# Performance work log

Measured on AMD Instinct MI355X. Metric: run time of the kernel, lower is better.

## Reference

```python
import jax, jax.numpy as jnp
import numpy as np

HEADS = 16
DIM_HEAD = 64
QUERY_DIM = 1024
CONTEXT_DIM = 1024
D_ATTN = HEADS * DIM_HEAD
SCALE = DIM_HEAD ** -0.5


def setup_inputs() -> dict:
    key = jax.random.key(0)
    ks = jax.random.split(key, 7)
    B, N, M = 4, 2048, 1024
    x = jax.random.normal(ks[0], (B, N, QUERY_DIM), dtype=jnp.float32)
    context = jax.random.normal(ks[1], (B, M, CONTEXT_DIM), dtype=jnp.float32)
    # Linear weights stored as [in, out] (no bias for Q/K/V, bias for to_out)
    s = 0.02
    Wq = jax.random.normal(ks[2], (QUERY_DIM, D_ATTN), dtype=jnp.float32) * s
    Wk = jax.random.normal(ks[3], (CONTEXT_DIM, D_ATTN), dtype=jnp.float32) * s
    Wv = jax.random.normal(ks[4], (CONTEXT_DIM, D_ATTN), dtype=jnp.float32) * s
    Wo = jax.random.normal(ks[5], (D_ATTN, QUERY_DIM), dtype=jnp.float32) * s
    bo = jax.random.normal(ks[6], (QUERY_DIM,), dtype=jnp.float32) * s
    return {"x": x, "context": context, "Wq": Wq, "Wk": Wk, "Wv": Wv, "Wo": Wo, "bo": bo}


def reference(x, context, Wq, Wk, Wv, Wo, bo):
    B, N, _ = x.shape
    M = context.shape[1]
    Q = (x @ Wq).reshape(B, N, HEADS, DIM_HEAD)        # b n h d
    K = (context @ Wk).reshape(B, M, HEADS, DIM_HEAD)  # b m h d
    V = (context @ Wv).reshape(B, M, HEADS, DIM_HEAD)
    # scores: b q h m  (matches torch einsum 'bqhd,bhmd->bqhm')
    scores = jnp.einsum('bqhd,bmhd->bqhm', Q, K) * SCALE
    attn = jax.nn.softmax(scores, axis=-1)
    out = jnp.einsum('bqhm,bmhd->bqhd', attn, V)
    out = out.reshape(B, N, D_ATTN)
    return out @ Wo + bo  # dropout p=0.0 -> identity
```

## Files before the change

### kernel.cpp

```cpp
#include <hip/hip_runtime.h>
#include <math.h>


#define HEADS 16
#define DHEAD 64
#define DM    1024
#define BQ    4
#define NQ    2048
#define MK    1024

typedef unsigned short u16;
typedef __attribute__((ext_vector_type(8))) short bf16x8;
typedef __attribute__((ext_vector_type(4))) float f32x4;
typedef __attribute__((ext_vector_type(16))) float f32x16;

__device__ __forceinline__ u16 f2bf(float f) {
  unsigned u = __builtin_bit_cast(unsigned, f);
  u = u + 0x7FFFu + ((u >> 16) & 1u);
  return (u16)(u >> 16);
}

__device__ __forceinline__ unsigned cvtpk(float lo, float hi2) {
  unsigned r;
  asm("v_cvt_pk_bf16_f32 %0, %1, %2" : "=v"(r) : "v"(lo), "v"(hi2));
  return r;
}

__device__ __forceinline__ float max3f(float a, float b, float c) {
  float d;
  asm("v_max3_f32 %0, %1, %2, %3" : "=v"(d) : "v"(a), "v"(b), "v"(c));
  return d;
}

__device__ __forceinline__ void gld16(const u16* g, u16* l) {
  __builtin_amdgcn_global_load_lds((const __attribute__((address_space(1))) void*)g,
                                   (__attribute__((address_space(3))) void*)l,
                                   16, 0, 0);
}

__global__ void k_cvt(const float* __restrict__ in, u16* __restrict__ out, int n8) {
  int i = blockIdx.x * 256 + threadIdx.x;
  if (i >= n8) return;
  float4 a = ((const float4*)in)[i * 2];
  float4 b = ((const float4*)in)[i * 2 + 1];
  union { u16 h[8]; int4 v; } r;
  r.h[0] = f2bf(a.x); r.h[1] = f2bf(a.y); r.h[2] = f2bf(a.z); r.h[3] = f2bf(a.w);
  r.h[4] = f2bf(b.x); r.h[5] = f2bf(b.y); r.h[6] = f2bf(b.z); r.h[7] = f2bf(b.w);
  ((int4*)out)[i] = r.v;
}

__global__ void k_wt(const float* __restrict__ W0, const float* __restrict__ W1,
                     const float* __restrict__ W2, const float* __restrict__ W3,
                     u16* __restrict__ out) {
  __shared__ float t[32][33];
  const float* W = blockIdx.z == 0 ? W0 : blockIdx.z == 1 ? W1 : blockIdx.z == 2 ? W2 : W3;
  u16* o = out + (size_t)blockIdx.z * DM * DM;
  int r0 = blockIdx.y * 32, c0 = blockIdx.x * 32;
  int tx = threadIdx.x, ty = threadIdx.y;
  for (int i = ty; i < 32; i += 8) t[i][tx] = W[(size_t)(r0 + i) * DM + c0 + tx];
  __syncthreads();
  for (int i = ty; i < 32; i += 8) o[(size_t)(c0 + i) * DM + r0 + tx] = f2bf(t[tx][i]);
}


#define VM6 asm volatile("s_waitcnt vmcnt(6)" ::: "memory")

#define STAGE_A8(bufi, h, kof) do {                                          \
  gld16(gA + (size_t)(h) * 131072 + (kof), &As8[bufi][(h) * 8192 + w * 512]); \
  gld16(gA + (size_t)(h) * 131072 + 65536 + (kof),                           \
        &As8[bufi][(h) * 8192 + 4096 + w * 512]);                            \
} while (0)

#define STAGE_B8(bufi, h, kof) do {                                          \
  gld16(gB + (size_t)(h) * 131072 + (kof), &Bs8[bufi][(h) * 8192 + w * 512]); \
  gld16(gB + (size_t)(h) * 131072 + 65536 + (kof),                           \
        &Bs8[bufi][(h) * 8192 + 4096 + w * 512]);                            \
} while (0)

#define RD_A8(qm) do { _Pragma("unroll")                                     \
  for (int mi = 0; mi < 4; ++mi) {                                           \
    const u16* pa = &As8[cur][((qm) * 128 + wmo + mi * 16 + lrow) * 64];     \
    af8[mi][0] = *(const bf16x8*)(pa + fo0);                                 \
    af8[mi][1] = *(const bf16x8*)(pa + (fo0 ^ 32));                          \
  } } while (0)

#define RD_B8(qn) do { _Pragma("unroll")                                     \
  for (int ni = 0; ni < 2; ++ni) {                                           \
    const u16* pb = &Bs8[cur][((qn) * 128 + wno + ni * 16 + lrow) * 64];     \
    bf8[ni][0] = *(const bf16x8*)(pb + fo0);                                 \
    bf8[ni][1] = *(const bf16x8*)(pb + (fo0 ^ 32));                          \
  } } while (0)

#define MM16(qm, qn) do {                                                    \
  __builtin_amdgcn_s_setprio(1);                                             \
  _Pragma("unroll")                                                          \
  for (int mi = 0; mi < 4; ++mi)                                             \
    _Pragma("unroll")                                                        \
    for (int ni = 0; ni < 2; ++ni) {                                         \
      acc[qm][qn][mi][ni] = __builtin_amdgcn_mfma_f32_16x16x32_bf16(         \
          af8[mi][0], bf8[ni][0], acc[qm][qn][mi][ni], 0, 0, 0);             \
      acc[qm][qn][mi][ni] = __builtin_amdgcn_mfma_f32_16x16x32_bf16(         \
          af8[mi][1], bf8[ni][1], acc[qm][qn][mi][ni], 0, 0, 0);             \
    }                                                                        \
  __builtin_amdgcn_s_setprio(0);                                             \
} while (0)

#define PH8(RDS, STG, VM, qm, qn) do {                                       \
  RDS;                                                                       \
  __builtin_amdgcn_sched_barrier(0);                                         \
  STG;                                                                       \
  VM;                                                                        \
  __builtin_amdgcn_s_barrier();                                              \
  asm volatile("s_waitcnt lgkmcnt(0)" ::: "memory");                         \
  __builtin_amdgcn_sched_barrier(0);                                         \
  MM16(qm, qn);                                                              \
  __builtin_amdgcn_sched_barrier(0);                                         \
  __builtin_amdgcn_s_barrier();                                              \
} while (0)

__global__ __launch_bounds__(512, 2) void k_gemm_qkv(const u16* __restrict__ xb,
                                                     const u16* __restrict__ cb,
                                                     const u16* __restrict__ wt,
                                                     u16* __restrict__ Qb,
                                                     u16* __restrict__ Kb,
                                                     u16* __restrict__ Vtb) {
  __shared__ u16 As8[2][16384];
  __shared__ u16 Bs8[2][16384];
  int lin = blockIdx.x;
  int swz = (lin & 7) * 32 + (lin >> 3);
  int p = swz >> 2, bx = swz & 3;
  const u16* A; const u16* Bt; u16* obf; int row0, mode;
  if (p < 32)      { A = xb; Bt = wt;           obf = Qb;  row0 = p * 256;        mode = 0; }
  else if (p < 48) { A = cb; Bt = wt + 1048576; obf = Kb;  row0 = (p - 32) * 256; mode = 0; }
  else             { A = cb; Bt = wt + 2097152; obf = Vtb; row0 = (p - 48) * 256; mode = 1; }
  int col0 = bx * 256;
  int t = threadIdx.x;
  int w = t >> 6, lane = t & 63, lrow = lane & 15, lgrp = lane >> 4;
  int wmo = (w >> 2) * 64, wno = (w & 3) * 32;
  int fo0 = (lgrp ^ (lrow & 7)) * 8;
  f32x4 acc[2][2][4][2] = {};
  bf16x8 af8[4][2], bf8[2][2];
  int srow = t >> 3, sunit = (t & 7) ^ ((t >> 3) & 7);
  const u16* gA = A  + (size_t)(row0 + srow) * DM + sunit * 8;
  const u16* gB = Bt + (size_t)(col0 + srow) * DM + sunit * 8;

  STAGE_A8(0, 0, 0);
  STAGE_B8(0, 1, 0);
  STAGE_B8(0, 0, 0);
  STAGE_A8(0, 1, 0);
  STAGE_A8(1, 0, 64);
  STAGE_B8(1, 1, 64);
  VM6;
  __syncthreads();

  #pragma unroll 2
  for (int u = 0; u < 16; ++u) {
    int cur = u & 1, nxt = cur ^ 1;
    int k1 = (u >= 15 ? 15 : u + 1) * 64;
    int k2 = (u >= 14 ? 15 : u + 2) * 64;
    PH8({ RD_A8(0); RD_B8(0); }, STAGE_B8(nxt, 0, k1), VM6,     0, 0);
    PH8({ RD_B8(1); },           STAGE_A8(nxt, 1, k1), (void)0, 0, 1);
    PH8({ RD_A8(1); },           STAGE_A8(cur, 0, k2), (void)0, 1, 1);
    PH8({ RD_B8(0); },           STAGE_B8(cur, 1, k2), VM6,     1, 0);
  }

  #pragma unroll
  for (int qm = 0; qm < 2; ++qm)
    #pragma unroll
    for (int qn = 0; qn < 2; ++qn)
      #pragma unroll
      for (int mi = 0; mi < 4; ++mi)
        #pragma unroll
        for (int ni = 0; ni < 2; ++ni)
          #pragma unroll
          for (int j = 0; j < 4; ++j) {
            int gr = row0 + qm * 128 + wmo + mi * 16 + lgrp * 4 + j;
            int gc = col0 + qn * 128 + wno + ni * 16 + lrow;
            float v = acc[qm][qn][mi][ni][j];
            if (mode == 0) {
              obf[(size_t)gr * DM + gc] = f2bf(v);
            } else {
              int b = gr >> 10, m = gr & 1023;
              obf[((size_t)(b * DM + gc)) * MK + m] = f2bf(v);
            }
          }
}

#define OSTG_A(bufi, h, kof) do {                                            \
  gld16(gA + (size_t)(h) * 131072 + (kof), &As8[bufi][(h) * 8192 + w * 512]); \
  gld16(gA + (size_t)(h) * 131072 + 65536 + (kof),                           \
        &As8[bufi][(h) * 8192 + 4096 + w * 512]);                            \
} while (0)

#define OSTG_B(bufi, h, kof)                                                 \
  gld16(gB + (size_t)(h) * 65536 + (kof), &Bs8[bufi][(h) * 4096 + w * 512])

#define ORD_A(qm) do { _Pragma("unroll")                                     \
  for (int mi = 0; mi < 2; ++mi) {                                           \
    const u16* pa = &As8[cur][((qm) * 128 + wmo + mi * 16 + lrow) * 64];     \
    af[mi][0] = *(const bf16x8*)(pa + fo0);                                  \
    af[mi][1] = *(const bf16x8*)(pa + (fo0 ^ 32));                           \
  } } while (0)

#define ORD_B(qn, dst) do { _Pragma("unroll")                                \
  for (int ni = 0; ni < 2; ++ni) {                                           \
    const u16* pb = &Bs8[cur][((qn) * 64 + wno + ni * 16 + lrow) * 64];      \
    dst[ni][0] = *(const bf16x8*)(pb + fo0);                                 \
    dst[ni][1] = *(const bf16x8*)(pb + (fo0 ^ 32));                          \
  } } while (0)

#define OMM(qm, qn, bfq) do {                                                \
  __builtin_amdgcn_s_setprio(1);                                             \
  _Pragma("unroll")                                                          \
  for (int mi = 0; mi < 2; ++mi)                                             \
    _Pragma("unroll")                                                        \
    for (int ni = 0; ni < 2; ++ni) {                                         \
      acc[qm][qn][mi][ni] = __builtin_amdgcn_mfma_f32_16x16x32_bf16(         \
          af[mi][0], bfq[ni][0], acc[qm][qn][mi][ni], 0, 0, 0);              \
      acc[qm][qn][mi][ni] = __builtin_amdgcn_mfma_f32_16x16x32_bf16(         \
          af[mi][1], bfq[ni][1], acc[qm][qn][mi][ni], 0, 0, 0);              \
    }                                                                        \
  __builtin_amdgcn_s_setprio(0);                                             \
} while (0)

#define OPH(RDS, STG, VM, qm, qn, bfq) do {                                  \
  RDS;                                                                       \
  __builtin_amdgcn_sched_barrier(0);                                         \
  STG;                                                                       \
  VM;                                                                        \
  __builtin_amdgcn_s_barrier();                                              \
  asm volatile("s_waitcnt lgkmcnt(0)" ::: "memory");                         \
  __builtin_amdgcn_sched_barrier(0);                                         \
  OMM(qm, qn, bfq);                                                          \
  __builtin_amdgcn_sched_barrier(0);                                         \
  __builtin_amdgcn_s_barrier();                                              \
} while (0)

__global__ __launch_bounds__(512, 2) void k_gemm_o(const u16* __restrict__ A,
                                                   const u16* __restrict__ Bt,
                                                   float* __restrict__ of32,
                                                   const float* __restrict__ bias) {
  __shared__ u16 As8[2][16384];
  __shared__ u16 Bs8[2][8192];
  int lin = blockIdx.x;
  int swz = (lin & 7) * 32 + (lin >> 3);
  int p = swz >> 3, bx = swz & 7;
  int row0 = p * 256, col0 = bx * 128;
  int t = threadIdx.x;
  int w = t >> 6, lane = t & 63, lrow = lane & 15, lgrp = lane >> 4;
  int wmo = (w >> 1) * 32, wno = (w & 1) * 32;
  int fo0 = (lgrp ^ (lrow & 7)) * 8;
  f32x4 acc[2][2][2][2] = {};
  bf16x8 af[2][2], bfA[2][2], bfB[2][2];
  int srow = t >> 3, sunit = (t & 7) ^ ((t >> 3) & 7);
  const u16* gA = A  + (size_t)(row0 + srow) * DM + sunit * 8;
  const u16* gB = Bt + (size_t)(col0 + srow) * DM + sunit * 8;

  OSTG_A(0, 0, 0);
  OSTG_B(0, 1, 0);
  OSTG_B(0, 0, 0);
  OSTG_A(0, 1, 0);
  OSTG_A(1, 0, 64);
  OSTG_B(1, 1, 64);
  asm volatile("s_waitcnt vmcnt(5)" ::: "memory");
  __syncthreads();

  #pragma unroll 2
  for (int u = 0; u < 16; ++u) {
    int cur = u & 1, nxt = cur ^ 1;
    int k1 = (u >= 15 ? 15 : u + 1) * 64;
    int k2 = (u >= 14 ? 15 : u + 2) * 64;
    OPH({ ORD_A(0); ORD_B(0, bfA); }, OSTG_B(nxt, 0, k1),
        asm volatile("s_waitcnt vmcnt(4)" ::: "memory"), 0, 0, bfA);
    OPH({ ORD_B(1, bfB); },           OSTG_A(nxt, 1, k1), (void)0, 0, 1, bfB);
    OPH({ ORD_A(1); },                OSTG_A(cur, 0, k2), (void)0, 1, 1, bfB);
    OPH({ (void)0; },                 OSTG_B(cur, 1, k2),
        asm volatile("s_waitcnt vmcnt(5)" ::: "memory"), 1, 0, bfA);
  }

  #pragma unroll
  for (int qm = 0; qm < 2; ++qm)
    #pragma unroll
    for (int qn = 0; qn < 2; ++qn)
      #pragma unroll
      for (int mi = 0; mi < 2; ++mi)
        #pragma unroll
        for (int ni = 0; ni < 2; ++ni)
          #pragma unroll
          for (int j = 0; j < 4; ++j) {
            int gr = row0 + qm * 128 + wmo + mi * 16 + lgrp * 4 + j;
            int gc = col0 + qn * 64 + wno + ni * 16 + lrow;
            of32[(size_t)gr * DM + gc] = acc[qm][qn][mi][ni][j] + bias[gc];
          }
}

#define BUILD_PFRAG(sv, base, frag) {                     \
  unsigned a_ = cvtpk(sv[base + 0], sv[base + 1]);        \
  unsigned c_ = cvtpk(sv[base + 2], sv[base + 3]);        \
  unsigned b_ = cvtpk(sv[base + 4], sv[base + 5]);        \
  unsigned d_ = cvtpk(sv[base + 6], sv[base + 7]);        \
  asm("v_permlane32_swap_b32 %0, %1" : "+v"(a_), "+v"(b_)); \
  asm("v_permlane32_swap_b32 %0, %1" : "+v"(c_), "+v"(d_)); \
  union { unsigned w[4]; bf16x8 v; } u_;                  \
  u_.w[0] = a_;  u_.w[1] = c_;                            \
  u_.w[2] = b_;  u_.w[3] = d_;                            \
  frag = u_.v; }

#define PV_CHUNK(sv, base, c) {                                               \
  bf16x8 pf_; BUILD_PFRAG(sv, base, pf_);                                     \
  int mo_ = ((c) * 16 + hi * 8) ^ sw;                                         \
  bf16x8 vf0_ = *(const bf16x8*)&Vl[cur][ln * 64 + mo_];                      \
  bf16x8 vf1_ = *(const bf16x8*)&Vl[cur][(32 + ln) * 64 + mo_];               \
  __builtin_amdgcn_s_setprio(1);                                              \
  o0 = __builtin_amdgcn_mfma_f32_32x32x16_bf16(vf0_, pf_, o0, 0, 0, 0);       \
  o1 = __builtin_amdgcn_mfma_f32_32x32x16_bf16(vf1_, pf_, o1, 0, 0, 0);       \
  __builtin_amdgcn_s_setprio(0); }

__device__ __forceinline__ float max16(const f32x16 &v) {
  float m0 = max3f(v[0], v[1], v[2]);
  float m1 = max3f(v[3], v[4], v[5]);
  float m2 = max3f(v[6], v[7], v[8]);
  float m3 = max3f(v[9], v[10], v[11]);
  float m4 = max3f(v[12], v[13], v[14]);
  float a = max3f(m0, m1, m2);
  float b = max3f(m3, m4, v[15]);
  return fmaxf(a, b);
}

__device__ __forceinline__ float sum16(const f32x16 &v) {
  float a = (v[0] + v[1]) + (v[2] + v[3]);
  float b = (v[4] + v[5]) + (v[6] + v[7]);
  float c = (v[8] + v[9]) + (v[10] + v[11]);
  float d = (v[12] + v[13]) + (v[14] + v[15]);
  return (a + b) + (c + d);
}

__global__ __launch_bounds__(512) void k_attn(const u16* __restrict__ Q,
                                              const u16* __restrict__ K,
                                              const u16* __restrict__ Vt,
                                              u16* __restrict__ O) {
  __shared__ __align__(16) u16 Kl[2][4096];
  __shared__ __align__(16) u16 Vl[2][4096];
  int bh = blockIdx.y, b = bh >> 4, h = bh & 15;
  int n0 = blockIdx.x * 256;
  int t = threadIdx.x, w = t >> 6, lane = t & 63;
  int ln = lane & 31, hi = lane >> 5;
  const float s2 = 0.18033688011112042f;

  int qrow = n0 + w * 32 + ln;
  const u16* qp = &Q[(((size_t)(b * NQ + qrow)) * HEADS + h) * DHEAD + hi * 8];
  bf16x8 qf0 = *(const bf16x8*)(qp);
  bf16x8 qf1 = *(const bf16x8*)(qp + 16);
  bf16x8 qf2 = *(const bf16x8*)(qp + 32);
  bf16x8 qf3 = *(const bf16x8*)(qp + 48);

  f32x16 o0 = {}, o1 = {};
  float M_ = -1e30f, L_ = 0.f;

  int srow = t >> 3, sp = (t & 7) * 8;
  const u16* kg = &K[(((size_t)(b * MK + srow)) * HEADS + h) * DHEAD + sp];
  const u16* vg = &Vt[((size_t)(b * DM) + h * DHEAD + srow) * MK + sp];
  int sd = srow * 64 + (sp ^ ((srow & 7) << 3));
  int sw = (ln & 7) << 3;

  int4 kv = *(const int4*)kg;
  int4 vv = *(const int4*)vg;
  *(int4*)&Kl[0][sd] = kv;
  *(int4*)&Vl[0][sd] = vv;
  __syncthreads();

  for (int it = 0; it < 16; ++it) {
    int cur = it & 1;
    if (it < 15) {
      kv = *(const int4*)(kg + (size_t)(it + 1) * (64 * HEADS * DHEAD));
      vv = *(const int4*)(vg + (it + 1) * 64);
    }

    f32x16 s0 = {}, s1 = {};
    __builtin_amdgcn_s_setprio(1);
    #pragma unroll
    for (int kd = 0; kd < 4; ++kd) {
      int doff = (kd * 16 + hi * 8) ^ sw;
      bf16x8 kf0 = *(const bf16x8*)&Kl[cur][ln * 64 + doff];
      bf16x8 kf1 = *(const bf16x8*)&Kl[cur][(32 + ln) * 64 + doff];
      bf16x8 qk = kd == 0 ? qf0 : kd == 1 ? qf1 : kd == 2 ? qf2 : qf3;
      s0 = __builtin_amdgcn_mfma_f32_32x32x16_bf16(kf0, qk, s0, 0, 0, 0);
      s1 = __builtin_amdgcn_mfma_f32_32x32x16_bf16(kf1, qk, s1, 0, 0, 0);
    }
    __builtin_amdgcn_s_setprio(0);

    float vm = fmaxf(max16(s0), max16(s1));

    if (!__all(vm - M_ <= 8.0f)) {
      float vm2 = fmaxf(vm, __shfl_xor(vm, 32));
      float mn = fmaxf(M_, vm2);
      float rc = exp2f((M_ - mn) * s2);
      M_ = mn;
      L_ *= rc;
      #pragma unroll
      for (int i = 0; i < 16; ++i) { o0[i] *= rc; o1[i] *= rc; }
    }
    float nb = M_ * s2;
    #pragma unroll
    for (int i = 0; i < 16; ++i) s0[i] = exp2f(s0[i] * s2 - nb);
    #pragma unroll
    for (int i = 0; i < 16; ++i) s1[i] = exp2f(s1[i] * s2 - nb);
    L_ += sum16(s0) + sum16(s1);

    PV_CHUNK(s0, 0, 0);
    PV_CHUNK(s0, 8, 1);
    PV_CHUNK(s1, 0, 2);
    PV_CHUNK(s1, 8, 3);

    if (it < 15) {
      *(int4*)&Kl[cur ^ 1][sd] = kv;
      *(int4*)&Vl[cur ^ 1][sd] = vv;
    }
    __syncthreads();
  }

  float Lt = L_ + __shfl_xor(L_, 32);
  float inv = 1.0f / Lt;
  u16* ob = (u16*)&O[(((size_t)(b * NQ + qrow)) * HEADS + h) * DHEAD];
  #pragma unroll
  for (int g = 0; g < 4; ++g) {
    union { u16 h4[4]; uint2 v; } r0, r1;
    #pragma unroll
    for (int s = 0; s < 4; ++s) {
      r0.h4[s] = f2bf(o0[4 * g + s] * inv);
      r1.h4[s] = f2bf(o1[4 * g + s] * inv);
    }
    *(uint2*)(ob + 8 * g + 4 * hi) = r0.v;
    *(uint2*)(ob + 32 + 8 * g + 4 * hi) = r1.v;
  }
}

extern "C" void kernel_launch(void* const* d_in, const int* in_sizes, int n_in,
                              void* d_out, int out_size, void* d_ws, size_t ws_size,
                              hipStream_t stream) {
  (void)in_sizes; (void)n_in; (void)out_size; (void)ws_size;
  const float* x   = (const float*)d_in[0];
  const float* ctx = (const float*)d_in[1];
  const float* Wq  = (const float*)d_in[2];
  const float* Wk  = (const float*)d_in[3];
  const float* Wv  = (const float*)d_in[4];
  const float* Wo  = (const float*)d_in[5];
  const float* bo  = (const float*)d_in[6];
  float* out = (float*)d_out;
  char* ws = (char*)d_ws;
  const size_t MB = 1u << 20;
  u16* xb  = (u16*)(ws);
  u16* cb  = (u16*)(ws + 16 * MB);
  u16* wt  = (u16*)(ws + 24 * MB);
  u16* Qb  = (u16*)(ws + 32 * MB);
  u16* Kb  = (u16*)(ws + 48 * MB);
  u16* Vtb = (u16*)(ws + 56 * MB);
  u16* Ab  = (u16*)(ws + 64 * MB);

  k_cvt<<<4096, 256, 0, stream>>>(x,   xb, 1048576);
  k_cvt<<<2048, 256, 0, stream>>>(ctx, cb, 524288);
  k_wt<<<dim3(32, 32, 4), dim3(32, 8), 0, stream>>>(Wq, Wk, Wv, Wo, wt);

  k_gemm_qkv<<<256, 512, 0, stream>>>(xb, cb, wt, Qb, Kb, Vtb);

  k_attn<<<dim3(8, 64), 512, 0, stream>>>(Qb, Kb, Vtb, Ab);

  k_gemm_o<<<256, 512, 0, stream>>>(Ab, wt + 3145728, out, bo);
}
```

Measured before the change: 164.1 us.

## Software-pipeline attention loop: overlap next QK with current softmax/PV, async LDS loads

Restructures the attention inner loop so the QK MFMA for tile i runs alongside the softmax and PV for tile i-1. V gets a triple-buffered LDS slot, and the loop is fully unrolled with two alternating score register sets. Global-to-LDS staging now goes through a gld16 helper (presumably direct global-to-LDS loads) with the swizzle moved to the global address side, so loads no longer pass through registers. The aim is to hide softmax latency behind matrix work and cut register-staged copies, at the cost of more registers and LDS.

Result: slower. 173.7 us (+5.9%).

```diff
diff --git a/kernel.cpp b/kernel.cpp
--- a/kernel.cpp
+++ b/kernel.cpp
@@ -306,11 +306,11 @@
   u_.w[2] = b_;  u_.w[3] = d_;                            \
   frag = u_.v; }
 
-#define PV_CHUNK(sv, base, c) {                                               \
+#define PV_CHUNK(sv, base, c, vb) {                                           \
   bf16x8 pf_; BUILD_PFRAG(sv, base, pf_);                                     \
   int mo_ = ((c) * 16 + hi * 8) ^ sw;                                         \
-  bf16x8 vf0_ = *(const bf16x8*)&Vl[cur][ln * 64 + mo_];                      \
-  bf16x8 vf1_ = *(const bf16x8*)&Vl[cur][(32 + ln) * 64 + mo_];               \
+  bf16x8 vf0_ = *(const bf16x8*)&Vl[vb][ln * 64 + mo_];                       \
+  bf16x8 vf1_ = *(const bf16x8*)&Vl[vb][(32 + ln) * 64 + mo_];                \
   __builtin_amdgcn_s_setprio(1);                                              \
   o0 = __builtin_amdgcn_mfma_f32_32x32x16_bf16(vf0_, pf_, o0, 0, 0, 0);       \
   o1 = __builtin_amdgcn_mfma_f32_32x32x16_bf16(vf1_, pf_, o1, 0, 0, 0);       \
@@ -335,12 +335,62 @@
   return (a + b) + (c + d);
 }
 
+#define STAGE_T(tile) do {                                        \
+  gld16(kgb + (size_t)(tile) * 65536, &Kl[(tile) & 1][w * 512]);  \
+  gld16(vgb + (tile) * 64,            &Vl[(tile) % 3][w * 512]);  \
+} while (0)
+
+#define QK_STEP(kb, S0, S1) do {                                           \
+  S0 = (f32x16){}; S1 = (f32x16){};                                        \
+  __builtin_amdgcn_s_setprio(1);                                           \
+  _Pragma("unroll")                                                        \
+  for (int kd = 0; kd < 4; ++kd) {                                         \
+    int doff = (kd * 16 + hi * 8) ^ sw;                                    \
+    bf16x8 kf0 = *(const bf16x8*)&Kl[kb][ln * 64 + doff];                  \
+    bf16x8 kf1 = *(const bf16x8*)&Kl[kb][(32 + ln) * 64 + doff];           \
+    bf16x8 qk = kd == 0 ? qf0 : kd == 1 ? qf1 : kd == 2 ? qf2 : qf3;       \
+    S0 = __builtin_amdgcn_mfma_f32_32x32x16_bf16(kf0, qk, S0, 0, 0, 0);    \
+    S1 = __builtin_amdgcn_mfma_f32_32x32x16_bf16(kf1, qk, S1, 0, 0, 0);    \
+  }                                                                        \
+  __builtin_amdgcn_s_setprio(0);                                           \
+} while (0)
+
+#define SMPV(S0, S1, vb) do {                                              \
+  float vm = fmaxf(max16(S0), max16(S1));                                  \
+  if (!__all(vm - M_ <= 8.0f)) {                                           \
+    float vm2 = fmaxf(vm, __shfl_xor(vm, 32));                             \
+    float mn = fmaxf(M_, vm2);                                             \
+    float rc = exp2f((M_ - mn) * s2);                                      \
+    M_ = mn;                                                               \
+    L_ *= rc;                                                              \
+    _Pragma("unroll")                                                      \
+    for (int i = 0; i < 16; ++i) { o0[i] *= rc; o1[i] *= rc; }             \
+  }                                                                        \
+  float nb = M_ * s2;                                                      \
+  _Pragma("unroll")                                                        \
+  for (int i = 0; i < 16; ++i) S0[i] = exp2f(S0[i] * s2 - nb);             \
+  _Pragma("unroll")                                                        \
+  for (int i = 0; i < 16; ++i) S1[i] = exp2f(S1[i] * s2 - nb);             \
+  L_ += sum16(S0) + sum16(S1);                                             \
+  PV_CHUNK(S0, 0, 0, vb);                                                  \
+  PV_CHUNK(S0, 8, 1, vb);                                                  \
+  PV_CHUNK(S1, 0, 2, vb);                                                  \
+  PV_CHUNK(S1, 8, 3, vb);                                                  \
+} while (0)
+
+#define AITER(it, SC0, SC1, SP0, SP1) do {                                 \
+  if ((it) < 15) STAGE_T((it) + 1);                                        \
+  QK_STEP((it) & 1, SC0, SC1);                                             \
+  SMPV(SP0, SP1, ((it) - 1) % 3);                                          \
+  __syncthreads();                                                         \
+} while (0)
+
 __global__ __launch_bounds__(512) void k_attn(const u16* __restrict__ Q,
                                               const u16* __restrict__ K,
                                               const u16* __restrict__ Vt,
                                               u16* __restrict__ O) {
   __shared__ __align__(16) u16 Kl[2][4096];
-  __shared__ __align__(16) u16 Vl[2][4096];
+  __shared__ __align__(16) u16 Vl[3][4096];
   int bh = blockIdx.y, b = bh >> 4, h = bh & 15;
   int n0 = blockIdx.x * 256;
   int t = threadIdx.x, w = t >> 6, lane = t & 63;
@@ -355,69 +405,36 @@
   bf16x8 qf3 = *(const bf16x8*)(qp + 48);
 
   f32x16 o0 = {}, o1 = {};
+  f32x16 sA0, sA1, sB0, sB1;
   float M_ = -1e30f, L_ = 0.f;
 
-  int srow = t >> 3, sp = (t & 7) * 8;
-  const u16* kg = &K[(((size_t)(b * MK + srow)) * HEADS + h) * DHEAD + sp];
-  const u16* vg = &Vt[((size_t)(b * DM) + h * DHEAD + srow) * MK + sp];
-  int sd = srow * 64 + (sp ^ ((srow & 7) << 3));
+  int srow = t >> 3, su = (t & 7) ^ ((t >> 3) & 7);
+  const u16* kgb = &K[(((size_t)(b * MK + srow)) * HEADS + h) * DHEAD + su * 8];
+  const u16* vgb = &Vt[((size_t)(b * DM) + h * DHEAD + srow) * MK + su * 8];
   int sw = (ln & 7) << 3;
 
-  int4 kv = *(const int4*)kg;
-  int4 vv = *(const int4*)vg;
-  *(int4*)&Kl[0][sd] = kv;
-  *(int4*)&Vl[0][sd] = vv;
+  STAGE_T(0);
   __syncthreads();
-
-  for (int it = 0; it < 16; ++it) {
-    int cur = it & 1;
-    if (it < 15) {
-      kv = *(const int4*)(kg + (size_t)(it + 1) * (64 * HEADS * DHEAD));
-      vv = *(const int4*)(vg + (it + 1) * 64);
-    }
-
-    f32x16 s0 = {}, s1 = {};
-    __builtin_amdgcn_s_setprio(1);
-    #pragma unroll
-    for (int kd = 0; kd < 4; ++kd) {
-      int doff = (kd * 16 + hi * 8) ^ sw;
-      bf16x8 kf0 = *(const bf16x8*)&Kl[cur][ln * 64 + doff];
-      bf16x8 kf1 = *(const bf16x8*)&Kl[cur][(32 + ln) * 64 + doff];
-      bf16x8 qk = kd == 0 ? qf0 : kd == 1 ? qf1 : kd == 2 ? qf2 : qf3;
-      s0 = __builtin_amdgcn_mfma_f32_32x32x16_bf16(kf0, qk, s0, 0, 0, 0);
-      s1 = __builtin_amdgcn_mfma_f32_32x32x16_bf16(kf1, qk, s1, 0, 0, 0);
-    }
-    __builtin_amdgcn_s_setprio(0);
-
-    float vm = fmaxf(max16(s0), max16(s1));
-
-    if (!__all(vm - M_ <= 8.0f)) {
-      float vm2 = fmaxf(vm, __shfl_xor(vm, 32));
-      float mn = fmaxf(M_, vm2);
-      float rc = exp2f((M_ - mn) * s2);
-      M_ = mn;
-      L_ *= rc;
-      #pragma unroll
-      for (int i = 0; i < 16; ++i) { o0[i] *= rc; o1[i] *= rc; }
-    }
-    float nb = M_ * s2;
-    #pragma unroll
-    for (int i = 0; i < 16; ++i) s0[i] = exp2f(s0[i] * s2 - nb);
-    #pragma unroll
-    for (int i = 0; i < 16; ++i) s1[i] = exp2f(s1[i] * s2 - nb);
-    L_ += sum16(s0) + sum16(s1);
-
-    PV_CHUNK(s0, 0, 0);
-    PV_CHUNK(s0, 8, 1);
-    PV_CHUNK(s1, 0, 2);
-    PV_CHUNK(s1, 8, 3);
-
-    if (it < 15) {
-      *(int4*)&Kl[cur ^ 1][sd] = kv;
-      *(int4*)&Vl[cur ^ 1][sd] = vv;
-    }
-    __syncthreads();
-  }
+  STAGE_T(1);
+  QK_STEP(0, sA0, sA1);
+  __syncthreads();
+
+  AITER(1,  sB0, sB1, sA0, sA1);
+  AITER(2,  sA0, sA1, sB0, sB1);
+  AITER(3,  sB0, sB1, sA0, sA1);
+  AITER(4,  sA0, sA1, sB0, sB1);
+  AITER(5,  sB0, sB1, sA0, sA1);
+  AITER(6,  sA0, sA1, sB0, sB1);
+  AITER(7,  sB0, sB1, sA0, sA1);
+  AITER(8,  sA0, sA1, sB0, sB1);
+  AITER(9,  sB0, sB1, sA0, sA1);
+  AITER(10, sA0, sA1, sB0, sB1);
+  AITER(11, sB0, sB1, sA0, sA1);
+  AITER(12, sA0, sA1, sB0, sB1);
+  AITER(13, sB0, sB1, sA0, sA1);
+  AITER(14, sA0, sA1, sB0, sB1);
+  AITER(15, sB0, sB1, sA0, sA1);
+  SMPV(sB0, sB1, 0);
 
   float Lt = L_ + __shfl_xor(L_, 32);
   float inv = 1.0f / Lt;
```
